# Kernel tuning notes

Hardware: AMD Instinct MI355X
Metric: run time of the kernel (lower is better)

## Reference

```python
import jax, jax.numpy as jnp
import numpy as np

H = 512        # num_hidden
Z = 512        # latent_len
TIME = 0.2
N_STEPS = 4    # fixed-step RK4 replaces adaptive dopri5 (same dynamics math)
B, N = 4, 4096


def _linear_params(k, fin, fout):
    k1, k2 = jax.random.split(k)
    s = 1.0 / np.sqrt(fin)
    W = jax.random.uniform(k1, (fout, fin), minval=-s, maxval=s, dtype=jnp.float32)
    b = jax.random.uniform(k2, (fout,), minval=-s, maxval=s, dtype=jnp.float32)
    return W, b


def setup_inputs() -> dict:
    key = jax.random.key(0)
    ks = jax.random.split(key, 16)
    inp = {
        "code": jax.random.normal(ks[0], (B, 1, Z), dtype=jnp.float32),
        "x": jax.random.uniform(ks[1], (B, N, 3), dtype=jnp.float32),
    }
    dims = {"l1": (3, H), "l2": (H, H), "l3": (H, H), "l4": (H, 3), "cond": (Z, H)}
    i = 2
    for f in ("f1", "f2"):
        for name, (fin, fout) in dims.items():
            W, b = _linear_params(ks[i], fin, fout)
            i += 1
            inp[f + "_" + name + "_w"] = W
            inp[f + "_" + name + "_b"] = b
    return inp


def _node_block(x, sf, W1, b1, W2, b2, W3, b3, W4, b4):
    """Fixed-step RK4 integration of ODEFunc dynamics over [0, TIME].
    x: (B,N,3) point state; sf: (B,1,H) precomputed tanh(cond(code)) shape features
    (constant along the trajectory since the latent code has zero dynamics)."""
    def dyn(p):
        pf = jax.nn.relu(p @ W1.T + b1)          # (B,N,H) point features
        h = pf * sf                               # gated point-shape features
        h = jax.nn.relu(h @ W2.T + b2) + h        # residual stage 1
        h = jax.nn.relu(h @ W3.T + b3) + h        # residual stage 2
        return jnp.tanh(h @ W4.T + b4)            # (B,N,3) flow direction

    dt = TIME / N_STEPS
    def step(p, _):
        k1 = dyn(p)
        k2 = dyn(p + 0.5 * dt * k1)
        k3 = dyn(p + 0.5 * dt * k2)
        k4 = dyn(p + dt * k3)
        return p + (dt / 6.0) * (k1 + 2.0 * k2 + 2.0 * k3 + k4), None

    x, _ = jax.lax.scan(step, x, None, length=N_STEPS)
    return x


def reference(code, x,
              f1_l1_w, f1_l1_b, f1_l2_w, f1_l2_b, f1_l3_w, f1_l3_b,
              f1_l4_w, f1_l4_b, f1_cond_w, f1_cond_b,
              f2_l1_w, f2_l1_b, f2_l2_w, f2_l2_b, f2_l3_w, f2_l3_b,
              f2_l4_w, f2_l4_b, f2_cond_w, f2_cond_b):
    sf1 = jnp.tanh(code @ f1_cond_w.T + f1_cond_b)  # (B,1,H), broadcasts over N
    x = _node_block(x, sf1, f1_l1_w, f1_l1_b, f1_l2_w, f1_l2_b,
                    f1_l3_w, f1_l3_b, f1_l4_w, f1_l4_b)
    sf2 = jnp.tanh(code @ f2_cond_w.T + f2_cond_b)
    x = _node_block(x, sf2, f2_l1_w, f2_l1_b, f2_l2_w, f2_l2_b,
                    f2_l3_w, f2_l3_b, f2_l4_w, f2_l4_b)
    return x  # pred_y: (B,N,3)
```

## Files before the change

kernel.cpp:

```cpp
#include <hip/hip_runtime.h>
#include <stdint.h>

typedef short short8 __attribute__((ext_vector_type(8)));
typedef unsigned short u16x4 __attribute__((ext_vector_type(4)));
typedef float floatx16 __attribute__((ext_vector_type(16)));

#define NPTS 16384
#define TILE_M 64
#define THREADS 1024
#define PA 2
#define PB 4

__device__ inline unsigned short f2bf(float f) {
  __bf16 h = (__bf16)f;
  return __builtin_bit_cast(unsigned short, h);
}
__device__ inline float bf2f(unsigned short h) {
  union { unsigned u; float f; } v; v.u = ((unsigned)h) << 16;
  return v.f;
}

__device__ inline void wave_stagger(int wid) {
  int steps = ((wid >> 2) & 3) * 4 + (wid & 3);
  for (int d = 0; d < steps; ++d)
    asm volatile("s_nop 7\n\ts_nop 7\n\ts_nop 7\n\ts_nop 7\n\ts_nop 7" :::);
}

__global__
__attribute__((amdgpu_flat_work_group_size(THREADS, THREADS),
               amdgpu_waves_per_eu(4, 4)))
void node_kernel(
    const float* __restrict__ x, float* __restrict__ outp,
    const unsigned short* __restrict__ wbf, const float* __restrict__ sfall,
    const float* __restrict__ w1a, const float* __restrict__ b1a,
    const float* __restrict__ b2a, const float* __restrict__ b3a,
    const float* __restrict__ w4a, const float* __restrict__ b4a,
    const float* __restrict__ w1b, const float* __restrict__ b1b,
    const float* __restrict__ b2b, const float* __restrict__ b3b,
    const float* __restrict__ w4b, const float* __restrict__ b4b)
{
  __shared__ unsigned short actA[TILE_M][520];
  __shared__ unsigned short actB2[TILE_M][520];
  __shared__ float pcur4[TILE_M][4];
  __shared__ float pev4[TILE_M][4];
  __shared__ float kac4[TILE_M][4];
  __shared__ float w4c[64][28];

  const int tid = threadIdx.x;
  const int wg = blockIdx.x;
  const int m0 = wg * TILE_M;
  const int batch = wg >> 6;
  const int lane = tid & 63;
  const int wid = tid >> 6;

  if (tid < TILE_M * 3) {
    int m = tid / 3, c = tid % 3;
    float v = x[m0 * 3 + tid];
    pcur4[m][c] = v;
    pev4[m][c] = v;
  }
  __syncthreads();

  const int aBase = (lane & 31) * 1040 + (lane >> 5) * 16;
  const int bcol = wid * 64 + lane;

  const int p1col = tid & 511;
  const int p1r0 = (tid >> 9) * 32;

  const int ep_m = lane & 31;
  const int ep_nb = wid * 32 + 4 * (lane >> 5);

  const float dt = 0.05f;

  #pragma unroll 1
  for (int f = 0; f < 2; ++f) {
    const float* w1 = f ? w1b : w1a;
    const float* b1v = f ? b1b : b1a;
    const float* b2v = f ? b2b : b2a;
    const float* b3v = f ? b3b : b3a;
    const float* w4 = f ? w4b : w4a;
    const float* b4v = f ? b4b : b4a;
    const short8* w2p = (const short8*)(wbf + (size_t)(f * 2 + 0) * 262144) + bcol;
    const short8* w3p = (const short8*)(wbf + (size_t)(f * 2 + 1) * 262144) + bcol;

    const float ww0 = w1[p1col * 3 + 0], ww1 = w1[p1col * 3 + 1], ww2 = w1[p1col * 3 + 2];
    const float bb = b1v[p1col];
    const float ss = sfall[f * 2048 + batch * 512 + p1col];
    const float b40 = b4v[0], b41 = b4v[1], b42 = b4v[2];

    for (int i = tid; i < 64 * 24; i += THREADS) {
      int q = i / 24, r = i % 24;
      w4c[q][r] = w4[(r >> 3) * 512 + q * 8 + (r & 7)];
    }
    __syncthreads();

    #pragma unroll 1
    for (int st = 0; st < 4; ++st) {
      #pragma unroll 1
      for (int stage = 0; stage < 4; ++stage) {
        short8 bq[PB];
        #pragma unroll
        for (int i = 0; i < PB - 1; ++i) bq[i] = w2p[i * 1024];

        #pragma unroll 4
        for (int mi = 0; mi < 32; ++mi) {
          int m = p1r0 + mi;
          const float4 pv = *(const float4*)&pev4[m][0];
          float v = fmaf(pv.x, ww0, fmaf(pv.y, ww1, fmaf(pv.z, ww2, bb)));
          v = fmaxf(v, 0.f) * ss;
          actA[m][p1col] = f2bf(v);
        }
        __syncthreads();

        #pragma unroll 1
        for (int s = 0; s < 2; ++s) {
          const float* bias = s ? b3v : b2v;
          const short8* bp = s ? w3p : w2p;
          const char* kb = s ? (const char*)&actB2[0][0] : (const char*)&actA[0][0];

          wave_stagger(wid);

          floatx16 acc0{}, acc1{};
          short8 aq0[PA], aq1[PA];
          #pragma unroll
          for (int i = 0; i < PA - 1; ++i) {
            aq0[i] = *(const short8*)(kb + aBase + i * 32);
            aq1[i] = *(const short8*)(kb + aBase + 33280 + i * 32);
          }

          #pragma unroll
          for (int kt = 0; kt < 32; ++kt) {
            int la = kt + PA - 1;
            if (la < 32) {
              aq0[la % PA] = *(const short8*)(kb + aBase + la * 32);
              aq1[la % PA] = *(const short8*)(kb + aBase + 33280 + la * 32);
            }
            int lb = kt + PB - 1;
            if (lb < 32) bq[lb % PB] = bp[lb * 1024];
            __builtin_amdgcn_s_setprio(1);
            acc0 = __builtin_amdgcn_mfma_f32_32x32x16_bf16(bq[kt % PB], aq0[kt % PA], acc0, 0, 0, 0);
            acc1 = __builtin_amdgcn_mfma_f32_32x32x16_bf16(bq[kt % PB], aq1[kt % PA], acc1, 0, 0, 0);
            __builtin_amdgcn_s_setprio(0);
          }

          if (s == 0) {
            #pragma unroll
            for (int i = 0; i < PB - 1; ++i) bq[i] = w3p[i * 1024];
          }

          {
            unsigned short (* __restrict__ wr)[520] = s ? actA : actB2;
            unsigned short (* __restrict__ rd)[520] = s ? actB2 : actA;
            #pragma unroll
            for (int g = 0; g < 4; ++g) {
              int n0 = ep_nb + 8 * g;
              const float4 bs = *(const float4*)&bias[n0];
              u16x4 r0 = *(const u16x4*)&rd[ep_m][n0];
              u16x4 r1 = *(const u16x4*)&rd[32 + ep_m][n0];
              u16x4 o0, o1;
              #pragma unroll
              for (int i = 0; i < 4; ++i) {
                float v = fmaxf(acc0[g * 4 + i] + ((const float*)&bs)[i], 0.f)
                          + bf2f((unsigned short)r0[i]);
                o0[i] = f2bf(v);
                v = fmaxf(acc1[g * 4 + i] + ((const float*)&bs)[i], 0.f)
                    + bf2f((unsigned short)r1[i]);
                o1[i] = f2bf(v);
              }
              *(u16x4*)&wr[ep_m][n0] = o0;
              *(u16x4*)&wr[32 + ep_m][n0] = o1;
            }
          }
          __syncthreads();
        }

        {
          int m = tid >> 4, jj = tid & 15;
          const unsigned short* arow = &actA[m][0];
          float s0 = 0.f, s1 = 0.f, s2 = 0.f;
          #pragma unroll
          for (int c = 0; c < 4; ++c) {
            int q = c * 16 + jj;
            int k0 = q * 8;
            short8 av = *(const short8*)(arow + k0);
            const float* wc = &w4c[q][0];
            #pragma unroll
            for (int half = 0; half < 2; ++half) {
              float4 wv0 = *(const float4*)(wc + 0 + half * 4);
              float4 wv1 = *(const float4*)(wc + 8 + half * 4);
              float4 wv2 = *(const float4*)(wc + 16 + half * 4);
              #pragma unroll
              for (int e = 0; e < 4; ++e) {
                float a = bf2f((unsigned short)av[half * 4 + e]);
                s0 = fmaf(a, ((const float*)&wv0)[e], s0);
                s1 = fmaf(a, ((const float*)&wv1)[e], s1);
                s2 = fmaf(a, ((const float*)&wv2)[e], s2);
              }
            }
          }
          s0 += __shfl_xor(s0, 1); s1 += __shfl_xor(s1, 1); s2 += __shfl_xor(s2, 1);
          s0 += __shfl_xor(s0, 2); s1 += __shfl_xor(s1, 2); s2 += __shfl_xor(s2, 2);
          s0 += __shfl_xor(s0, 4); s1 += __shfl_xor(s1, 4); s2 += __shfl_xor(s2, 4);
          s0 += __shfl_xor(s0, 8); s1 += __shfl_xor(s1, 8); s2 += __shfl_xor(s2, 8);
          if (jj < 3) {
            float sv = (jj == 0) ? s0 : ((jj == 1) ? s1 : s2);
            float bv = (jj == 0) ? b40 : ((jj == 1) ? b41 : b42);
            float fl = tanhf(sv + bv);
            float pc = pcur4[m][jj];
            if (stage == 0) {
              kac4[m][jj] = fl;
              pev4[m][jj] = fmaf(0.5f * dt, fl, pc);
            } else if (stage == 1) {
              kac4[m][jj] += 2.f * fl;
              pev4[m][jj] = fmaf(0.5f * dt, fl, pc);
            } else if (stage == 2) {
              kac4[m][jj] += 2.f * fl;
              pev4[m][jj] = fmaf(dt, fl, pc);
            } else {
              float np = fmaf(dt / 6.f, kac4[m][jj] + fl, pc);
              pcur4[m][jj] = np;
              pev4[m][jj] = np;
            }
          }
        }
        __syncthreads();
      }
    }
  }

  if (tid < TILE_M * 3) outp[m0 * 3 + tid] = pcur4[tid / 3][tid % 3];
}

__global__ void setup_shuffle(const float* s0, const float* s1, const float* s2,
                              const float* s3, unsigned short* dst) {
  int idx = blockIdx.x * blockDim.x + threadIdx.x;
  int w = idx >> 15;
  int r = idx & 32767;
  int lane = r & 63;
  int tile = r >> 6;
  int nt = tile & 15, kt = tile >> 4;
  const float* W = (w == 0) ? s0 : (w == 1) ? s1 : (w == 2) ? s2 : s3;
  int n = nt * 32 + (lane & 31);
  int k0 = kt * 16 + (lane >> 5) * 8;
  const float* src = W + n * 512 + k0;
  unsigned short* d = dst + ((size_t)w << 18) + (size_t)r * 8;
  #pragma unroll
  for (int j = 0; j < 8; ++j) d[j] = f2bf(src[j]);
}

__global__ void setup_sf(const float* code, const float* cw1, const float* cb1,
                         const float* cw2, const float* cb2, float* sfout) {
  int f = blockIdx.x >> 2, b = blockIdx.x & 3;
  const float* cw = f ? cw2 : cw1;
  const float* cb = f ? cb2 : cb1;
  int j = threadIdx.x;
  const float* c = code + b * 512;
  float s = cb[j];
  for (int k = 0; k < 512; ++k) s = fmaf(c[k], cw[j * 512 + k], s);
  sfout[f * 2048 + b * 512 + j] = tanhf(s);
}

extern "C" void kernel_launch(void* const* d_in, const int* in_sizes, int n_in,
                              void* d_out, int out_size, void* d_ws, size_t ws_size,
                              hipStream_t stream) {
  const float* code = (const float*)d_in[0];
  const float* x    = (const float*)d_in[1];
  char* ws = (char*)d_ws;
  float* sf = (float*)ws;
  unsigned short* wbf = (unsigned short*)(ws + 16384);

  setup_shuffle<<<512, 256, 0, stream>>>((const float*)d_in[4], (const float*)d_in[6],
                                         (const float*)d_in[14], (const float*)d_in[16], wbf);
  setup_sf<<<8, 512, 0, stream>>>(code, (const float*)d_in[10], (const float*)d_in[11],
                                  (const float*)d_in[20], (const float*)d_in[21], sf);

  node_kernel<<<NPTS / TILE_M, THREADS, 0, stream>>>(x, (float*)d_out, wbf, sf,
      (const float*)d_in[2], (const float*)d_in[3], (const float*)d_in[5],
      (const float*)d_in[7], (const float*)d_in[8], (const float*)d_in[9],
      (const float*)d_in[12], (const float*)d_in[13], (const float*)d_in[15],
      (const float*)d_in[17], (const float*)d_in[18], (const float*)d_in[19]);
}
```

Baseline: 754.2 us.

## Fuse final 512x3 projection into second residual GEMM epilogue

Unrolls the two-stage residual GEMM loop into two explicit blocks. The second block's epilogue now does the W4 projection directly from MFMA accumulators instead of writing the activation back to LDS and re-reading it. Per-wave partial sums are reduced across half-waves with shuffles, stored into a shared partial buffer, then summed across the 16 waves by 192 threads before tanh and the RK4 update. This drops one LDS write/read pass over the 64x512 tile. In exchange it adds a cross-wave reduction buffer and more registers in the epilogue.

```diff
diff --git a/kernel.cpp b/kernel.cpp
--- a/kernel.cpp
+++ b/kernel.cpp
@@ -44,7 +44,8 @@
   __shared__ float pcur4[TILE_M][4];
   __shared__ float pev4[TILE_M][4];
   __shared__ float kac4[TILE_M][4];
-  __shared__ float w4c[64][28];
+  __shared__ float w4t[512][4];
+  __shared__ float part[TILE_M][49];
 
   const int tid = threadIdx.x;
   const int wg = blockIdx.x;
@@ -88,9 +89,9 @@
     const float ss = sfall[f * 2048 + batch * 512 + p1col];
     const float b40 = b4v[0], b41 = b4v[1], b42 = b4v[2];
 
-    for (int i = tid; i < 64 * 24; i += THREADS) {
-      int q = i / 24, r = i % 24;
-      w4c[q][r] = w4[(r >> 3) * 512 + q * 8 + (r & 7)];
+    for (int i = tid; i < 2048; i += THREADS) {
+      int col = i >> 2, c = i & 3;
+      w4t[col][c] = (c < 3) ? w4[c * 512 + col] : 0.f;
     }
     __syncthreads();
 
@@ -112,14 +113,10 @@
         }
         __syncthreads();
 
-        #pragma unroll 1
-        for (int s = 0; s < 2; ++s) {
-          const float* bias = s ? b3v : b2v;
-          const short8* bp = s ? w3p : w2p;
-          const char* kb = s ? (const char*)&actB2[0][0] : (const char*)&actA[0][0];
-
+        {
+          const float* bias = b2v;
+          const char* kb = (const char*)&actA[0][0];
           wave_stagger(wid);
-
           floatx16 acc0{}, acc1{};
           short8 aq0[PA], aq1[PA];
           #pragma unroll
@@ -127,7 +124,6 @@
             aq0[i] = *(const short8*)(kb + aBase + i * 32);
             aq1[i] = *(const short8*)(kb + aBase + 33280 + i * 32);
           }
-
           #pragma unroll
           for (int kt = 0; kt < 32; ++kt) {
             int la = kt + PA - 1;
@@ -136,91 +132,121 @@
               aq1[la % PA] = *(const short8*)(kb + aBase + 33280 + la * 32);
             }
             int lb = kt + PB - 1;
-            if (lb < 32) bq[lb % PB] = bp[lb * 1024];
+            if (lb < 32) bq[lb % PB] = w2p[lb * 1024];
             __builtin_amdgcn_s_setprio(1);
             acc0 = __builtin_amdgcn_mfma_f32_32x32x16_bf16(bq[kt % PB], aq0[kt % PA], acc0, 0, 0, 0);
             acc1 = __builtin_amdgcn_mfma_f32_32x32x16_bf16(bq[kt % PB], aq1[kt % PA], acc1, 0, 0, 0);
             __builtin_amdgcn_s_setprio(0);
           }
-
-          if (s == 0) {
+          #pragma unroll
+          for (int i = 0; i < PB - 1; ++i) bq[i] = w3p[i * 1024];
+
+          #pragma unroll
+          for (int g = 0; g < 4; ++g) {
+            int n0 = ep_nb + 8 * g;
+            const float4 bs = *(const float4*)&bias[n0];
+            u16x4 r0 = *(const u16x4*)&actA[ep_m][n0];
+            u16x4 r1 = *(const u16x4*)&actA[32 + ep_m][n0];
+            u16x4 o0, o1;
             #pragma unroll
-            for (int i = 0; i < PB - 1; ++i) bq[i] = w3p[i * 1024];
-          }
-
-          {
-            unsigned short (* __restrict__ wr)[520] = s ? actA : actB2;
-            unsigned short (* __restrict__ rd)[520] = s ? actB2 : actA;
+            for (int i = 0; i < 4; ++i) {
+              float v = fmaxf(acc0[g * 4 + i] + ((const float*)&bs)[i], 0.f)
+                        + bf2f((unsigned short)r0[i]);
+              o0[i] = f2bf(v);
+              v = fmaxf(acc1[g * 4 + i] + ((const float*)&bs)[i], 0.f)
+                  + bf2f((unsigned short)r1[i]);
+              o1[i] = f2bf(v);
+            }
+            *(u16x4*)&actB2[ep_m][n0] = o0;
+            *(u16x4*)&actB2[32 + ep_m][n0] = o1;
+          }
+        }
+        __syncthreads();
+
+        {
+          const float* bias = b3v;
+          const char* kb = (const char*)&actB2[0][0];
+          wave_stagger(wid);
+          floatx16 acc0{}, acc1{};
+          short8 aq0[PA], aq1[PA];
+          #pragma unroll
+          for (int i = 0; i < PA - 1; ++i) {
+            aq0[i] = *(const short8*)(kb + aBase + i * 32);
+            aq1[i] = *(const short8*)(kb + aBase + 33280 + i * 32);
+          }
+          #pragma unroll
+          for (int kt = 0; kt < 32; ++kt) {
+            int la = kt + PA - 1;
+            if (la < 32) {
+              aq0[la % PA] = *(const short8*)(kb + aBase + la * 32);
+              aq1[la % PA] = *(const short8*)(kb + aBase + 33280 + la * 32);
+            }
+            int lb = kt + PB - 1;
+            if (lb < 32) bq[lb % PB] = w3p[lb * 1024];
+            __builtin_amdgcn_s_setprio(1);
+            acc0 = __builtin_amdgcn_mfma_f32_32x32x16_bf16(bq[kt % PB], aq0[kt % PA], acc0, 0, 0, 0);
+            acc1 = __builtin_amdgcn_mfma_f32_32x32x16_bf16(bq[kt % PB], aq1[kt % PA], acc1, 0, 0, 0);
+            __builtin_amdgcn_s_setprio(0);
+          }
+
+          float s00 = 0.f, s01 = 0.f, s02 = 0.f, s10 = 0.f, s11 = 0.f, s12 = 0.f;
+          #pragma unroll
+          for (int g = 0; g < 4; ++g) {
+            int n0 = ep_nb + 8 * g;
+            const float4 bs = *(const float4*)&bias[n0];
+            u16x4 r0 = *(const u16x4*)&actB2[ep_m][n0];
+            u16x4 r1 = *(const u16x4*)&actB2[32 + ep_m][n0];
             #pragma unroll
-            for (int g = 0; g < 4; ++g) {
-              int n0 = ep_nb + 8 * g;
-              const float4 bs = *(const float4*)&bias[n0];
-              u16x4 r0 = *(const u16x4*)&rd[ep_m][n0];
-              u16x4 r1 = *(const u16x4*)&rd[32 + ep_m][n0];
-              u16x4 o0, o1;
-              #pragma unroll
-              for (int i = 0; i < 4; ++i) {
-                float v = fmaxf(acc0[g * 4 + i] + ((const float*)&bs)[i], 0.f)
-                          + bf2f((unsigned short)r0[i]);
-                o0[i] = f2bf(v);
-                v = fmaxf(acc1[g * 4 + i] + ((const float*)&bs)[i], 0.f)
-                    + bf2f((unsigned short)r1[i]);
-                o1[i] = f2bf(v);
-              }
-              *(u16x4*)&wr[ep_m][n0] = o0;
-              *(u16x4*)&wr[32 + ep_m][n0] = o1;
+            for (int i = 0; i < 4; ++i) {
+              const float4 wv = *(const float4*)&w4t[n0 + i][0];
+              float v = fmaxf(acc0[g * 4 + i] + ((const float*)&bs)[i], 0.f)
+                        + bf2f((unsigned short)r0[i]);
+              float h = bf2f(f2bf(v));
+              s00 = fmaf(h, wv.x, s00);
+              s01 = fmaf(h, wv.y, s01);
+              s02 = fmaf(h, wv.z, s02);
+              v = fmaxf(acc1[g * 4 + i] + ((const float*)&bs)[i], 0.f)
+                  + bf2f((unsigned short)r1[i]);
+              h = bf2f(f2bf(v));
+              s10 = fmaf(h, wv.x, s10);
+              s11 = fmaf(h, wv.y, s11);
+              s12 = fmaf(h, wv.z, s12);
             }
           }
-          __syncthreads();
+          s00 += __shfl_xor(s00, 32); s01 += __shfl_xor(s01, 32); s02 += __shfl_xor(s02, 32);
+          s10 += __shfl_xor(s10, 32); s11 += __shfl_xor(s11, 32); s12 += __shfl_xor(s12, 32);
+          if (lane < 32) {
+            part[ep_m][wid * 3 + 0] = s00;
+            part[ep_m][wid * 3 + 1] = s01;
+            part[ep_m][wid * 3 + 2] = s02;
+            part[32 + ep_m][wid * 3 + 0] = s10;
+            part[32 + ep_m][wid * 3 + 1] = s11;
+            part[32 + ep_m][wid * 3 + 2] = s12;
+          }
         }
-
-        {
-          int m = tid >> 4, jj = tid & 15;
-          const unsigned short* arow = &actA[m][0];
-          float s0 = 0.f, s1 = 0.f, s2 = 0.f;
-          #pragma unroll
-          for (int c = 0; c < 4; ++c) {
-            int q = c * 16 + jj;
-            int k0 = q * 8;
-            short8 av = *(const short8*)(arow + k0);
-            const float* wc = &w4c[q][0];
-            #pragma unroll
-            for (int half = 0; half < 2; ++half) {
-              float4 wv0 = *(const float4*)(wc + 0 + half * 4);
-              float4 wv1 = *(const float4*)(wc + 8 + half * 4);
-              float4 wv2 = *(const float4*)(wc + 16 + half * 4);
-              #pragma unroll
-              for (int e = 0; e < 4; ++e) {
-                float a = bf2f((unsigned short)av[half * 4 + e]);
-                s0 = fmaf(a, ((const float*)&wv0)[e], s0);
-                s1 = fmaf(a, ((const float*)&wv1)[e], s1);
-                s2 = fmaf(a, ((const float*)&wv2)[e], s2);
-              }
-            }
-          }
-          s0 += __shfl_xor(s0, 1); s1 += __shfl_xor(s1, 1); s2 += __shfl_xor(s2, 1);
-          s0 += __shfl_xor(s0, 2); s1 += __shfl_xor(s1, 2); s2 += __shfl_xor(s2, 2);
-          s0 += __shfl_xor(s0, 4); s1 += __shfl_xor(s1, 4); s2 += __shfl_xor(s2, 4);
-          s0 += __shfl_xor(s0, 8); s1 += __shfl_xor(s1, 8); s2 += __shfl_xor(s2, 8);
-          if (jj < 3) {
-            float sv = (jj == 0) ? s0 : ((jj == 1) ? s1 : s2);
-            float bv = (jj == 0) ? b40 : ((jj == 1) ? b41 : b42);
-            float fl = tanhf(sv + bv);
-            float pc = pcur4[m][jj];
-            if (stage == 0) {
-              kac4[m][jj] = fl;
-              pev4[m][jj] = fmaf(0.5f * dt, fl, pc);
-            } else if (stage == 1) {
-              kac4[m][jj] += 2.f * fl;
-              pev4[m][jj] = fmaf(0.5f * dt, fl, pc);
-            } else if (stage == 2) {
-              kac4[m][jj] += 2.f * fl;
-              pev4[m][jj] = fmaf(dt, fl, pc);
-            } else {
-              float np = fmaf(dt / 6.f, kac4[m][jj] + fl, pc);
-              pcur4[m][jj] = np;
-              pev4[m][jj] = np;
-            }
+        __syncthreads();
+
+        if (tid < TILE_M * 3) {
+          int m = tid / 3, c = tid % 3;
+          float sum = 0.f;
+          #pragma unroll
+          for (int w = 0; w < 16; ++w) sum += part[m][w * 3 + c];
+          float bv = (c == 0) ? b40 : ((c == 1) ? b41 : b42);
+          float fl = tanhf(sum + bv);
+          float pc = pcur4[m][c];
+          if (stage == 0) {
+            kac4[m][c] = fl;
+            pev4[m][c] = fmaf(0.5f * dt, fl, pc);
+          } else if (stage == 1) {
+            kac4[m][c] += 2.f * fl;
+            pev4[m][c] = fmaf(0.5f * dt, fl, pc);
+          } else if (stage == 2) {
+            kac4[m][c] += 2.f * fl;
+            pev4[m][c] = fmaf(dt, fl, pc);
+          } else {
+            float np = fmaf(dt / 6.f, kac4[m][c] + fl, pc);
+            pcur4[m][c] = np;
+            pev4[m][c] = np;
           }
         }
         __syncthreads();
```

New measurement: 1.119 ms. 48.4% more time.
